# Kernel tuning notes

Hardware: AMD Instinct MI355X
Metric: run time of the kernel (lower is better)

## Reference

```python
import jax, jax.numpy as jnp
import numpy as np

N_E = 1024
E_DIM = 256
BETA = 0.25
BATCH = 131072


def setup_inputs() -> dict:
    key = jax.random.key(0)
    k1, k2 = jax.random.split(key)
    z = jax.random.normal(k1, (BATCH, E_DIM), dtype=jnp.float32)
    # matches nn.Embedding init uniform_(-1/n_e, 1/n_e)
    emb_weight = jax.random.uniform(k2, (N_E, E_DIM), dtype=jnp.float32,
                                    minval=-1.0 / N_E, maxval=1.0 / N_E)
    return {"z": z, "emb_weight": emb_weight}


def reference(z, emb_weight):
    # z: [B, e_dim] (the module's unsqueeze/permute/view is an identity reshape)
    # squared L2 distances: [B, n_e]
    d = (jnp.sum(z * z, axis=1, keepdims=True)
         + jnp.sum(emb_weight * emb_weight, axis=1)
         - 2.0 * jnp.matmul(z, emb_weight.T))
    min_encoding_indices = jnp.argmin(d, axis=1)            # [B]
    min_encodings = jax.nn.one_hot(min_encoding_indices, N_E, dtype=z.dtype)  # [B, n_e]
    z_q = jnp.matmul(min_encodings, emb_weight)             # [B, e_dim]

    sg = jax.lax.stop_gradient
    loss = jnp.mean((sg(z_q) - z) ** 2) + BETA * jnp.mean((z_q - sg(z)) ** 2)

    # straight-through estimator
    z_q_ste = z + sg(z_q - z)

    e_mean = jnp.mean(min_encodings, axis=0)                # [n_e]
    perplexity = jnp.exp(-jnp.sum(e_mean * jnp.log(e_mean + 1e-10)))

    return (z_q_ste, loss, min_encoding_indices[:, None], perplexity)
```

## Files before the change

kernel.cpp:

```cpp
#include <hip/hip_runtime.h>

typedef __attribute__((ext_vector_type(8))) __bf16 bf16x8;
typedef __attribute__((ext_vector_type(4))) float f32x4;
typedef __attribute__((ext_vector_type(8))) unsigned short u16x8;

#define B_ROWS 131072
#define EDIM   256
#define N_E    1024
#define BMR    64
#define CHUNKS 32
#define CAP    16
#define OROWS  32

#define OUT1 ((size_t)B_ROWS * EDIM)
#define OUT2 (OUT1 + 1)
#define OUT3 (OUT2 + B_ROWS)
#define SCR_WORDS 10

#define WS_EMBT  0
#define WS_ESQ   524288
#define WS_COUNT 528384
#define WS_LOSS  532480

__device__ __forceinline__ unsigned short f2bf(float f) {
    unsigned u = __float_as_uint(f);
    return (unsigned short)((u + 0x7FFFu + ((u >> 16) & 1u)) >> 16);
}
__device__ __forceinline__ unsigned encf(float f) {
    unsigned u = __float_as_uint(f);
    return u ^ (unsigned)(((int)u >> 31) | 0x80000000);
}
__device__ __forceinline__ float decf(unsigned x) {
    return (x & 0x80000000u) ? __uint_as_float(x ^ 0x80000000u)
                             : __uint_as_float(~x);
}
__device__ __forceinline__ float med3f(float a, float b, float c) {
#if __has_builtin(__builtin_amdgcn_fmed3f)
    return __builtin_amdgcn_fmed3f(a, b, c);
#else
    return fmaxf(fminf(a, b), fminf(fmaxf(a, b), c));
#endif
}

__device__ inline float pw128_sq(const float* p) {
    float4 v0 = *(const float4*)p, v1 = *(const float4*)(p + 4);
    float r[8];
    r[0] = __fmul_rn(v0.x, v0.x); r[1] = __fmul_rn(v0.y, v0.y);
    r[2] = __fmul_rn(v0.z, v0.z); r[3] = __fmul_rn(v0.w, v0.w);
    r[4] = __fmul_rn(v1.x, v1.x); r[5] = __fmul_rn(v1.y, v1.y);
    r[6] = __fmul_rn(v1.z, v1.z); r[7] = __fmul_rn(v1.w, v1.w);
    for (int i = 8; i < 128; i += 8) {
        v0 = *(const float4*)(p + i); v1 = *(const float4*)(p + i + 4);
        r[0] = __fadd_rn(r[0], __fmul_rn(v0.x, v0.x));
        r[1] = __fadd_rn(r[1], __fmul_rn(v0.y, v0.y));
        r[2] = __fadd_rn(r[2], __fmul_rn(v0.z, v0.z));
        r[3] = __fadd_rn(r[3], __fmul_rn(v0.w, v0.w));
        r[4] = __fadd_rn(r[4], __fmul_rn(v1.x, v1.x));
        r[5] = __fadd_rn(r[5], __fmul_rn(v1.y, v1.y));
        r[6] = __fadd_rn(r[6], __fmul_rn(v1.z, v1.z));
        r[7] = __fadd_rn(r[7], __fmul_rn(v1.w, v1.w));
    }
    float s01 = __fadd_rn(r[0], r[1]), s23 = __fadd_rn(r[2], r[3]);
    float s45 = __fadd_rn(r[4], r[5]), s67 = __fadd_rn(r[6], r[7]);
    return __fadd_rn(__fadd_rn(s01, s23), __fadd_rn(s45, s67));
}

__device__ inline float exact_d(const float* zp, const float* ep, float zsq, float eq) {
    const float4* z4 = (const float4*)zp;
    const float4* e4 = (const float4*)ep;
    float acc = 0.f;
#pragma unroll 8
    for (int k = 0; k < 64; ++k) {
        float4 a = z4[k], b = e4[k];
        acc = __fmaf_rn(a.x, b.x, acc);
        acc = __fmaf_rn(a.y, b.y, acc);
        acc = __fmaf_rn(a.z, b.z, acc);
        acc = __fmaf_rn(a.w, b.w, acc);
    }
    return __fsub_rn(__fadd_rn(zsq, eq), 2.0f * acc);
}

__global__ void prep_emb(const float* __restrict__ emb,
                         unsigned short* __restrict__ embT,
                         float* __restrict__ esqg)
{
    int n = blockIdx.x, t = threadIdx.x;
    const float4 v = ((const float4*)(emb + (size_t)n * EDIM))[t];
    ushort4 o = { f2bf(v.x), f2bf(v.y), f2bf(v.z), f2bf(v.w) };
    int g = t >> 1, j0 = (t & 1) * 4;
    *(ushort4*)(embT + ((size_t)g * N_E + n) * 8 + j0) = o;
    if (t < 2) {
        float h = pw128_sq(emb + (size_t)n * EDIM + 128 * t);
        float ho = __shfl_xor(h, 1);
        if (t == 0) esqg[n] = __fadd_rn(h, ho);
    }
}

#define INS(s_, code_, r_)                                                  \
    {                                                                       \
        bool lt1 = (s_) < bd1[r_];                                          \
        bool lt2 = (s_) < bd2[r_];                                          \
        bd3[r_] = med3f((s_), bd2[r_], bd3[r_]);                            \
        bd2[r_] = med3f((s_), bd1[r_], bd2[r_]);                            \
        bd1[r_] = fminf((s_), bd1[r_]);                                     \
        int low_ = cp_[r_] & 0xFFFF;                                        \
        cp_[r_] = lt1 ? ((code_) | (low_ << 16))                            \
                      : (lt2 ? (low_ | ((code_) << 16)) : cp_[r_]);         \
    }

__global__ __launch_bounds__(256, 4) void vq_scan(
    const float* __restrict__ z, const unsigned short* __restrict__ embT,
    const float* __restrict__ esqg, float* __restrict__ out)
{
    __shared__ float esq_s[N_E];
    __shared__ float S_s[BMR];
    __shared__ unsigned cnt[BMR];
    __shared__ unsigned short list[BMR][CAP];

    const int tid  = threadIdx.x;
    const int blk  = blockIdx.x;
    const int lane = tid & 63;
    const int w    = tid >> 6;
    const int col  = lane & 15;
    const int quad = lane >> 4;
    const int row0 = w * 16;

    const float* zb = z + (size_t)blk * BMR * EDIM;

    for (int i = tid; i < N_E; i += 256) esq_s[i] = esqg[i];
    if (tid < BMR) cnt[tid] = 0u;

    bf16x8 afr[8];
    {
        int row = row0 + col;
#pragma unroll
        for (int ks = 0; ks < 8; ++ks) {
            const float* p = zb + row * EDIM + ((ks * 4 + quad) << 3);
            float4 a0 = *(const float4*)p;
            float4 a1 = *(const float4*)(p + 4);
            u16x8 t = { f2bf(a0.x), f2bf(a0.y), f2bf(a0.z), f2bf(a0.w),
                        f2bf(a1.x), f2bf(a1.y), f2bf(a1.z), f2bf(a1.w) };
            afr[ks] = *(bf16x8*)&t;
        }
    }

    if (tid < 128) {
        int row = tid >> 1, half = tid & 1;
        const float4* p4 = (const float4*)(zb + row * EDIM + half * 128);
        float4 sv = {0.f, 0.f, 0.f, 0.f};
#pragma unroll
        for (int jj = 0; jj < 32; ++jj) {
            float4 vv = p4[jj];
            sv.x += fabsf(vv.x); sv.y += fabsf(vv.y);
            sv.z += fabsf(vv.z); sv.w += fabsf(vv.w);
        }
        float sa = (sv.x + sv.y) + (sv.z + sv.w);
        float so = __shfl_xor(sa, 1);
        if (half == 0) S_s[row] = (sa + so) * 1.001f;
    }
    __syncthreads();

    int koff[8];
#pragma unroll
    for (int ks = 0; ks < 8; ++ks)
        koff[ks] = ((((ks * 4 + quad) << 10) + col) << 3);

    float bd1[4], bd2[4], bd3[4];
    int   cp_[4];
#pragma unroll
    for (int r = 0; r < 4; ++r) {
        bd1[r] = INFINITY; bd2[r] = INFINITY; bd3[r] = INFINITY; cp_[r] = 0;
    }

    for (int c = 0; c < CHUNKS; ++c) {
        const unsigned short* cb = embT + (c << 8);
        {
            u16x8 bfr[8];
#pragma unroll
            for (int ks = 0; ks < 8; ++ks)
                bfr[ks] = *(const u16x8*)(cb + koff[ks]);
            f32x4 acc = {0.f, 0.f, 0.f, 0.f};
#pragma unroll
            for (int ks = 0; ks < 8; ++ks)
                acc = __builtin_amdgcn_mfma_f32_16x16x32_bf16(afr[ks], *(bf16x8*)&bfr[ks], acc, 0, 0, 0);
            const int codeN = (c << 5) + col;
            const float eqv = esq_s[codeN];
#pragma unroll
            for (int r = 0; r < 4; ++r) {
                float s = __fmaf_rn(-2.0f, acc[r], eqv);
                INS(s, codeN, r);
            }
        }
        {
            u16x8 bfr[8];
#pragma unroll
            for (int ks = 0; ks < 8; ++ks)
                bfr[ks] = *(const u16x8*)(cb + koff[ks] + 128);
            f32x4 acc = {0.f, 0.f, 0.f, 0.f};
#pragma unroll
            for (int ks = 0; ks < 8; ++ks)
                acc = __builtin_amdgcn_mfma_f32_16x16x32_bf16(afr[ks], *(bf16x8*)&bfr[ks], acc, 0, 0, 0);
            const int codeN = (c << 5) + 16 + col;
            const float eqv = esq_s[codeN];
#pragma unroll
            for (int r = 0; r < 4; ++r) {
                float s = __fmaf_rn(-2.0f, acc[r], eqv);
                INS(s, codeN, r);
            }
        }
    }

    float th[4];
#pragma unroll
    for (int r = 0; r < 4; ++r) {
        unsigned long long kk =
            ((unsigned long long)encf(bd1[r]) << 32) | (unsigned)(cp_[r] & 0xFFFF);
#pragma unroll
        for (int msk = 1; msk <= 8; msk <<= 1) {
            unsigned long long o = __shfl_xor(kk, msk);
            if (o < kk) kk = o;
        }
        int row = row0 + quad * 4 + r;
        th[r] = decf((unsigned)(kk >> 32)) + (S_s[row] * (1.0f / 131072.0f) + 1e-4f);
    }

#pragma unroll
    for (int r = 0; r < 4; ++r) {
        int row = row0 + quad * 4 + r;
        if (__builtin_expect(bd1[r] <= th[r], 0)) {
            unsigned i = atomicAdd(&cnt[row], 1u);
            if (i < CAP) list[row][i] = (unsigned short)(cp_[r] & 0xFFFF);
        }
        if (__builtin_expect(bd2[r] <= th[r], 0)) {
            unsigned i = atomicAdd(&cnt[row], 1u);
            if (i < CAP) list[row][i] = (unsigned short)((unsigned)cp_[r] >> 16);
        }
        if (__builtin_expect(bd3[r] <= th[r], 0))
            atomicAdd(&cnt[row], 1000u);
    }
    __syncthreads();

    if (tid < BMR) {
        unsigned* rec = (unsigned*)out + ((size_t)blk * BMR + tid) * SCR_WORDS;
        rec[0] = cnt[tid];
#pragma unroll
        for (int k = 0; k < 8; ++k)
            rec[1 + k] = (unsigned)list[tid][2 * k] | ((unsigned)list[tid][2 * k + 1] << 16);
    }
}

__global__ void vq_rescore(
    const float* __restrict__ z, const float* __restrict__ emb,
    const float* __restrict__ esqg, float* __restrict__ out,
    unsigned int* __restrict__ count)
{
    __shared__ float esq_s[N_E];
    __shared__ float zsq_s[BMR];
    __shared__ int rowbest[BMR];
    __shared__ unsigned long long fb4[4];

    const int tid  = threadIdx.x;
    const int blk  = blockIdx.x;
    const int lane = tid & 63;
    const int w    = tid >> 6;
    const float* zb = z + (size_t)blk * BMR * EDIM;

    for (int i = tid; i < N_E; i += 256) esq_s[i] = esqg[i];
    __syncthreads();

    {
        int row = tid >> 2, j = tid & 3;
        const float* zrow = zb + row * EDIM;
        float h = (j < 2) ? pw128_sq(zrow + 128 * j) : 0.f;
        int base = lane & ~3;
        float v0 = __shfl(h, base);
        float v1 = __shfl(h, base + 1);
        float zq = __fadd_rn(v0, v1);
        if (j == 0) zsq_s[row] = zq;

        const unsigned* rec = (const unsigned*)out + ((size_t)blk * BMR + row) * SCR_WORDS;
        int cn = (int)rec[0];
        unsigned long long bkey = ~0ull;
        if (cn <= CAP) {
            for (int i = j; i < cn; i += 4) {
                unsigned pr = rec[1 + (i >> 1)];
                int n = (int)((i & 1) ? (pr >> 16) : (pr & 0xFFFF));
                float d = exact_d(zrow, emb + (size_t)n * EDIM, zq, esq_s[n]);
                unsigned long long k2 = ((unsigned long long)encf(d) << 32) | (unsigned)n;
                if (k2 < bkey) bkey = k2;
            }
        }
#pragma unroll
        for (int m = 1; m <= 2; m <<= 1) {
            unsigned long long o = __shfl_xor(bkey, m);
            if (o < bkey) bkey = o;
        }
        if (j == 0) rowbest[row] = (cn <= CAP) ? (int)(bkey & 0xFFFFFFFFu) : -1;
    }
    __syncthreads();

    for (int r = 0; r < BMR; ++r) {
        if (rowbest[r] != -1) continue;
        const float* zr = zb + r * EDIM;
        float zqr = zsq_s[r];
        unsigned long long k = ~0ull;
        for (int ci = 0; ci < 4; ++ci) {
            int n = tid + ci * 256;
            float d = exact_d(zr, emb + (size_t)n * EDIM, zqr, esq_s[n]);
            unsigned long long k2 = ((unsigned long long)encf(d) << 32) | (unsigned)n;
            if (k2 < k) k = k2;
        }
#pragma unroll
        for (int msk = 1; msk <= 32; msk <<= 1) {
            unsigned long long o = __shfl_xor(k, msk);
            if (o < k) k = o;
        }
        if (lane == 0) fb4[w] = k;
        __syncthreads();
        if (tid == 0) {
            unsigned long long m0 = fb4[0] < fb4[1] ? fb4[0] : fb4[1];
            unsigned long long m1 = fb4[2] < fb4[3] ? fb4[2] : fb4[3];
            rowbest[r] = (int)((m0 < m1 ? m0 : m1) & 0xFFFFFFFFu);
        }
        __syncthreads();
    }

    if (tid < BMR) {
        int bn = rowbest[tid];
        out[OUT2 + (size_t)blk * BMR + tid] = (float)bn;
        atomicAdd(&count[bn], 1u);
    }
}

__global__ void vq_output(const float* __restrict__ z, const float* __restrict__ emb,
                          float* __restrict__ out, double* __restrict__ lossSum)
{
    __shared__ double red4s[4];
    const int tid = threadIdx.x;
    const int blk = blockIdx.x;
    const int lane = tid & 63;
    const int w   = tid >> 6;
    const int row = tid >> 3;
    const int q   = tid & 7;
    const size_t grow = (size_t)blk * OROWS + row;
    const int bn = (int)out[OUT2 + grow];
    const float4* zp4 = (const float4*)(z + grow * EDIM);
    const float4* ebr = (const float4*)(emb + (size_t)bn * EDIM);
    float4* outr = (float4*)(out + grow * EDIM);
    double lacc = 0.0;
#pragma unroll
    for (int i = 0; i < 8; ++i) {
        int k4 = q + i * 8;
        float4 zv = zp4[k4];
        float4 ev = ebr[k4];
        float4 o; float sd;
        sd = __fsub_rn(ev.x, zv.x); o.x = __fadd_rn(zv.x, sd); lacc += (double)__fmul_rn(sd, sd);
        sd = __fsub_rn(ev.y, zv.y); o.y = __fadd_rn(zv.y, sd); lacc += (double)__fmul_rn(sd, sd);
        sd = __fsub_rn(ev.z, zv.z); o.z = __fadd_rn(zv.z, sd); lacc += (double)__fmul_rn(sd, sd);
        sd = __fsub_rn(ev.w, zv.w); o.w = __fadd_rn(zv.w, sd); lacc += (double)__fmul_rn(sd, sd);
        outr[k4] = o;
    }
#pragma unroll
    for (int msk = 1; msk <= 32; msk <<= 1) lacc += __shfl_xor(lacc, msk);
    if (lane == 0) red4s[w] = lacc;
    __syncthreads();
    if (tid == 0) atomicAdd(lossSum, red4s[0] + red4s[1] + red4s[2] + red4s[3]);
}

__global__ void vq_finalize(const unsigned int* __restrict__ count,
                            const double* __restrict__ lossSum,
                            float* __restrict__ out)
{
    __shared__ double red[1024];
    int t = threadIdx.x;
    double em = (double)count[t] * (1.0 / 131072.0);
    red[t] = em * log(em + 1e-10);
    __syncthreads();
    for (int s = 512; s > 0; s >>= 1) {
        if (t < s) red[t] += red[t + s];
        __syncthreads();
    }
    if (t == 0) {
        out[OUT3] = (float)exp(-red[0]);
        double m = lossSum[0] * (1.0 / 33554432.0);
        out[OUT1] = (float)(1.25 * m);
    }
}

extern "C" void kernel_launch(void* const* d_in, const int* in_sizes, int n_in,
                              void* d_out, int out_size, void* d_ws, size_t ws_size,
                              hipStream_t stream) {
    const float* z   = (const float*)d_in[0];
    const float* emb = (const float*)d_in[1];
    float* out = (float*)d_out;

    unsigned short* embT = (unsigned short*)((char*)d_ws + WS_EMBT);
    float* esqg          = (float*)((char*)d_ws + WS_ESQ);
    unsigned int* count  = (unsigned int*)((char*)d_ws + WS_COUNT);
    double* lossSum      = (double*)((char*)d_ws + WS_LOSS);

    hipMemsetAsync((char*)d_ws + WS_COUNT, 0, 4104, stream);
    prep_emb<<<N_E, 64, 0, stream>>>(emb, embT, esqg);
    vq_scan<<<B_ROWS / BMR, 256, 0, stream>>>(z, embT, esqg, out);
    vq_rescore<<<B_ROWS / BMR, 256, 0, stream>>>(z, emb, esqg, out, count);
    vq_output<<<B_ROWS / OROWS, 256, 0, stream>>>(z, emb, out, lossSum);
    vq_finalize<<<1, 1024, 0, stream>>>(count, lossSum, out);
}
```

Baseline: 391.1 us.

## Resolve single-candidate rows in scan and stagger codebook chunk order

The scan kernel now writes the index and bumps the histogram directly when a row has exactly one candidate within the bf16 error threshold. The rescore kernel then skips those rows entirely, including the z-row norm computation and its global reads. The fallback path now computes the row norm on demand inside the loop, at the cost of an extra barrier. Each wave also starts its codebook sweep at a different chunk offset, meant to spread L2/cache accesses across the embT buffer and avoid every block hitting the same lines together.

```diff
diff --git a/kernel.cpp b/kernel.cpp
--- a/kernel.cpp
+++ b/kernel.cpp
@@ -110,7 +110,8 @@
 
 __global__ __launch_bounds__(256, 4) void vq_scan(
     const float* __restrict__ z, const unsigned short* __restrict__ embT,
-    const float* __restrict__ esqg, float* __restrict__ out)
+    const float* __restrict__ esqg, float* __restrict__ out,
+    unsigned int* __restrict__ count)
 {
     __shared__ float esq_s[N_E];
     __shared__ float S_s[BMR];
@@ -124,6 +125,7 @@
     const int col  = lane & 15;
     const int quad = lane >> 4;
     const int row0 = w * 16;
+    const int coff = ((blk << 2) | w) & 31;
 
     const float* zb = z + (size_t)blk * BMR * EDIM;
 
@@ -173,7 +175,8 @@
     }
 
     for (int c = 0; c < CHUNKS; ++c) {
-        const unsigned short* cb = embT + (c << 8);
+        const int cc = (c + coff) & 31;
+        const unsigned short* cb = embT + (cc << 8);
         {
             u16x8 bfr[8];
 #pragma unroll
@@ -183,7 +186,7 @@
 #pragma unroll
             for (int ks = 0; ks < 8; ++ks)
                 acc = __builtin_amdgcn_mfma_f32_16x16x32_bf16(afr[ks], *(bf16x8*)&bfr[ks], acc, 0, 0, 0);
-            const int codeN = (c << 5) + col;
+            const int codeN = (cc << 5) + col;
             const float eqv = esq_s[codeN];
 #pragma unroll
             for (int r = 0; r < 4; ++r) {
@@ -200,7 +203,7 @@
 #pragma unroll
             for (int ks = 0; ks < 8; ++ks)
                 acc = __builtin_amdgcn_mfma_f32_16x16x32_bf16(afr[ks], *(bf16x8*)&bfr[ks], acc, 0, 0, 0);
-            const int codeN = (c << 5) + 16 + col;
+            const int codeN = (cc << 5) + 16 + col;
             const float eqv = esq_s[codeN];
 #pragma unroll
             for (int r = 0; r < 4; ++r) {
@@ -241,11 +244,20 @@
     __syncthreads();
 
     if (tid < BMR) {
-        unsigned* rec = (unsigned*)out + ((size_t)blk * BMR + tid) * SCR_WORDS;
-        rec[0] = cnt[tid];
-#pragma unroll
-        for (int k = 0; k < 8; ++k)
-            rec[1 + k] = (unsigned)list[tid][2 * k] | ((unsigned)list[tid][2 * k + 1] << 16);
+        int row = tid;
+        unsigned cn = cnt[row];
+        unsigned* rec = (unsigned*)out + ((size_t)blk * BMR + row) * SCR_WORDS;
+        rec[0] = cn;
+        if (cn == 1u) {
+            int bn = (int)list[row][0];
+            out[OUT2 + (size_t)blk * BMR + row] = (float)bn;
+            atomicAdd(&count[bn], 1u);
+        } else if (cn <= CAP) {
+#pragma unroll
+            for (int k = 0; k < 8; ++k)
+                rec[1 + k] = (unsigned)list[row][2 * k]
+                           | ((unsigned)list[row][2 * k + 1] << 16);
+        }
     }
 }
 
@@ -255,8 +267,8 @@
     unsigned int* __restrict__ count)
 {
     __shared__ float esq_s[N_E];
-    __shared__ float zsq_s[BMR];
     __shared__ int rowbest[BMR];
+    __shared__ float zq_fb;
     __shared__ unsigned long long fb4[4];
 
     const int tid  = threadIdx.x;
@@ -270,18 +282,18 @@
 
     {
         int row = tid >> 2, j = tid & 3;
-        const float* zrow = zb + row * EDIM;
-        float h = (j < 2) ? pw128_sq(zrow + 128 * j) : 0.f;
-        int base = lane & ~3;
-        float v0 = __shfl(h, base);
-        float v1 = __shfl(h, base + 1);
-        float zq = __fadd_rn(v0, v1);
-        if (j == 0) zsq_s[row] = zq;
-
         const unsigned* rec = (const unsigned*)out + ((size_t)blk * BMR + row) * SCR_WORDS;
         int cn = (int)rec[0];
-        unsigned long long bkey = ~0ull;
-        if (cn <= CAP) {
+        if (cn > CAP) {
+            if (j == 0) rowbest[row] = -1;
+        } else if (cn >= 2) {
+            const float* zrow = zb + row * EDIM;
+            float h = (j < 2) ? pw128_sq(zrow + 128 * j) : 0.f;
+            int base = lane & ~3;
+            float v0 = __shfl(h, base);
+            float v1 = __shfl(h, base + 1);
+            float zq = __fadd_rn(v0, v1);
+            unsigned long long bkey = ~0ull;
             for (int i = j; i < cn; i += 4) {
                 unsigned pr = rec[1 + (i >> 1)];
                 int n = (int)((i & 1) ? (pr >> 16) : (pr & 0xFFFF));
@@ -289,20 +301,30 @@
                 unsigned long long k2 = ((unsigned long long)encf(d) << 32) | (unsigned)n;
                 if (k2 < bkey) bkey = k2;
             }
-        }
-#pragma unroll
-        for (int m = 1; m <= 2; m <<= 1) {
-            unsigned long long o = __shfl_xor(bkey, m);
-            if (o < bkey) bkey = o;
-        }
-        if (j == 0) rowbest[row] = (cn <= CAP) ? (int)(bkey & 0xFFFFFFFFu) : -1;
+#pragma unroll
+            for (int m = 1; m <= 2; m <<= 1) {
+                unsigned long long o = __shfl_xor(bkey, m);
+                if (o < bkey) bkey = o;
+            }
+            if (j == 0) {
+                int bn = (int)(bkey & 0xFFFFFFFFu);
+                out[OUT2 + (size_t)blk * BMR + row] = (float)bn;
+                atomicAdd(&count[bn], 1u);
+                rowbest[row] = -2;
+            }
+        } else {
+            if (j == 0) rowbest[row] = -2;
+        }
     }
     __syncthreads();
 
     for (int r = 0; r < BMR; ++r) {
         if (rowbest[r] != -1) continue;
         const float* zr = zb + r * EDIM;
-        float zqr = zsq_s[r];
+        if (tid == 0)
+            zq_fb = __fadd_rn(pw128_sq(zr), pw128_sq(zr + 128));
+        __syncthreads();
+        float zqr = zq_fb;
         unsigned long long k = ~0ull;
         for (int ci = 0; ci < 4; ++ci) {
             int n = tid + ci * 256;
@@ -320,15 +342,11 @@
         if (tid == 0) {
             unsigned long long m0 = fb4[0] < fb4[1] ? fb4[0] : fb4[1];
             unsigned long long m1 = fb4[2] < fb4[3] ? fb4[2] : fb4[3];
-            rowbest[r] = (int)((m0 < m1 ? m0 : m1) & 0xFFFFFFFFu);
+            int bn = (int)((m0 < m1 ? m0 : m1) & 0xFFFFFFFFu);
+            out[OUT2 + (size_t)blk * BMR + r] = (float)bn;
+            atomicAdd(&count[bn], 1u);
         }
         __syncthreads();
-    }
-
-    if (tid < BMR) {
-        int bn = rowbest[tid];
-        out[OUT2 + (size_t)blk * BMR + tid] = (float)bn;
-        atomicAdd(&count[bn], 1u);
     }
 }
 
@@ -401,7 +419,7 @@
 
     hipMemsetAsync((char*)d_ws + WS_COUNT, 0, 4104, stream);
     prep_emb<<<N_E, 64, 0, stream>>>(emb, embT, esqg);
-    vq_scan<<<B_ROWS / BMR, 256, 0, stream>>>(z, embT, esqg, out);
+    vq_scan<<<B_ROWS / BMR, 256, 0, stream>>>(z, embT, esqg, out, count);
     vq_rescore<<<B_ROWS / BMR, 256, 0, stream>>>(z, emb, esqg, out, count);
     vq_output<<<B_ROWS / OROWS, 256, 0, stream>>>(z, emb, out, lossSum);
     vq_finalize<<<1, 1024, 0, stream>>>(count, lossSum, out);
```

Result: faster. 365.3 us (-6.6%).
